# Kernel tuning notes

Hardware: AMD Instinct MI355X
Metric: run time of the kernel (lower is better)

The kernel has to match this reference:

```python
import jax, jax.numpy as jnp
import numpy as np


def _bilinear_grid_sample(fea, grid):
    """torch.nn.functional.grid_sample, mode=bilinear, padding_mode=zeros, align_corners=False.
    fea: (B,C,H,W); grid: (B,Hg,Wg,2) with xy in [-1,1]. Returns (B,C,Hg,Wg)."""
    B, C, H, W = fea.shape
    Hg, Wg = grid.shape[1], grid.shape[2]
    gx, gy = grid[..., 0], grid[..., 1]
    # unnormalize (align_corners=False)
    x = ((gx + 1.0) * W - 1.0) * 0.5
    y = ((gy + 1.0) * H - 1.0) * 0.5
    x0 = jnp.floor(x); y0 = jnp.floor(y)
    x1 = x0 + 1.0;     y1 = y0 + 1.0
    wx1 = x - x0; wx0 = 1.0 - wx1
    wy1 = y - y0; wy0 = 1.0 - wy1
    flat = fea.reshape(B, C, H * W)

    def corner(xi, yi, w):
        valid = (xi >= 0) & (xi <= W - 1) & (yi >= 0) & (yi <= H - 1)
        xi_c = jnp.clip(xi, 0, W - 1).astype(jnp.int32)
        yi_c = jnp.clip(yi, 0, H - 1).astype(jnp.int32)
        idx = (yi_c * W + xi_c).reshape(B, 1, Hg * Wg)
        v = jnp.take_along_axis(flat, jnp.broadcast_to(idx, (B, C, Hg * Wg)), axis=2)
        return v * (w * valid.astype(fea.dtype)).reshape(B, 1, Hg * Wg)

    out = (corner(x0, y0, wx0 * wy0) + corner(x1, y0, wx1 * wy0)
           + corner(x0, y1, wx0 * wy1) + corner(x1, y1, wx1 * wy1))
    return out.reshape(B, C, Hg, Wg)


def _conv1d_k1(x, W, b):
    # x: (B,Cin,N), W: (Cout,Cin), b: (Cout,) -> (B,Cout,N)
    return jnp.einsum('oc,bcn->bon', W, x) + b[None, :, None]


def setup_inputs() -> dict:
    key = jax.random.key(0)
    ks = jax.random.split(key, 8)
    B, C, H, W = 4, 16, 90, 160
    N_s, N_anchor, N_y = 8, 200, 20
    scale = 8
    fea = jax.random.normal(ks[0], (B, C, H, W), dtype=jnp.float32)
    sampled_3d_points = jax.random.normal(ks[1], (N_s, B, N_anchor, N_y, 4), dtype=jnp.float32)
    # 2D pixel coords at full resolution: x in [0, W*scale), y in [0, H*scale)
    u = jax.random.uniform(ks[2], (N_s, B, N_anchor, N_y, 2), dtype=jnp.float32)
    points_2d_coord = u * jnp.array([W * scale, H * scale], dtype=jnp.float32)
    W_local = jax.random.normal(ks[3], (16, 16), dtype=jnp.float32) * 0.25
    b_local = jax.random.normal(ks[4], (16,), dtype=jnp.float32) * 0.01
    W_emb = jax.random.normal(ks[5], (256, 4), dtype=jnp.float32) * 0.5
    b_emb = jax.random.normal(ks[6], (256,), dtype=jnp.float32) * 0.01
    return {"fea": fea, "sampled_3d_points": sampled_3d_points,
            "points_2d_coord": points_2d_coord,
            "W_local": W_local, "b_local": b_local,
            "W_emb": W_emb, "b_emb": b_emb, "scale": scale}


def reference(fea, sampled_3d_points, points_2d_coord, W_local, b_local, W_emb, b_emb, scale):
    B, C, H, W = fea.shape
    N_s, _, N_anchor, N_y, _ = points_2d_coord.shape
    # normalize 2D coords to [-1,1] grid
    norm_weight = jnp.array([1.0 / W, 1.0 / H], dtype=fea.dtype)
    ner = (points_2d_coord / scale) * norm_weight * 2.0 - 1.0
    ner = jnp.transpose(ner, (1, 0, 2, 3, 4)).reshape(B, N_s * N_anchor, N_y, 2)
    local_fea = _bilinear_grid_sample(fea, ner)            # (B,C,N_s*N_anchor,N_y)
    local_fea = local_fea.reshape(B, C, -1)                # (B,C,N)
    local_fea = _conv1d_k1(local_fea, W_local, b_local)    # (B,16,N)
    # point embedding: permute(1,4,0,2,3) -> (B,4,N_s,N_anchor,N_y)
    sp = jnp.transpose(sampled_3d_points, (1, 4, 0, 2, 3)).reshape(B, 4, -1)
    embedded_points = _conv1d_k1(sp, W_emb, b_emb)         # (B,256,N)
    return (embedded_points, local_fea)
```

## Files before the change

kernel.cpp:

```cpp
#include <hip/hip_runtime.h>

#define B_    4
#define C_    16
#define H_    90
#define W_    160
#define NS_   8
#define NA_   200
#define NY_   20
#define NPB_  (NS_*NA_*NY_)
#define NPB4_ (NPB_/4)
#define CO_   256
#define EMB_ELEMS ((size_t)B_*CO_*NPB_)
#define SCALE_F 8.0f
#define HW_   (H_*W_)

__global__ __launch_bounds__(256) void fused_local_emb_kernel(
    const float*  __restrict__ fea,
    const float4* __restrict__ sp3d,
    const float2* __restrict__ pc2d,
    const float*  __restrict__ W_local,
    const float*  __restrict__ b_local,
    const float4* __restrict__ W_emb,
    const float*  __restrict__ b_emb,
    float* __restrict__ out)
{
    __shared__ float4 sWe[CO_];
    __shared__ float  sbe[CO_];
    __shared__ float  sWl[256];
    __shared__ float  sbl[16];
    __shared__ float  sPx[256], sPy[256], sPz[256], sPw[256];
    __shared__ float  sV[16*256];

    const int tid = threadIdx.x;
    sWe[tid] = W_emb[tid];
    sbe[tid] = b_emb[tid];
    sWl[tid] = W_local[tid];
    if (tid < 16) sbl[tid] = b_local[tid];

    const int blk  = blockIdx.x;
    const int b    = blk / (NPB_/256);
    const int tile = blk % (NPB_/256);
    const int n    = tile*256 + tid;

    const int s   = n / (NA_*NY_);
    const int rem = n - s*(NA_*NY_);
    const int a   = rem / NY_;
    const int yy  = rem - a*NY_;

    const int pidx = ((s*B_ + b)*NA_ + a)*NY_ + yy;
    const float4 p  = sp3d[pidx];
    const float2 pc = pc2d[pidx];

    sPx[tid] = p.x; sPy[tid] = p.y; sPz[tid] = p.z; sPw[tid] = p.w;

    const float gx = (pc.x / SCALE_F) * (1.0f/(float)W_) * 2.0f - 1.0f;
    const float gy = (pc.y / SCALE_F) * (1.0f/(float)H_) * 2.0f - 1.0f;
    const float xf = ((gx + 1.0f) * (float)W_ - 1.0f) * 0.5f;
    const float yf = ((gy + 1.0f) * (float)H_ - 1.0f) * 0.5f;

    const float x0f = floorf(xf), y0f = floorf(yf);
    const float x1f = x0f + 1.0f, y1f = y0f + 1.0f;
    const float wx1 = xf - x0f, wx0 = 1.0f - wx1;
    const float wy1 = yf - y0f, wy0 = 1.0f - wy1;

    const float vx0 = (x0f >= 0.0f && x0f <= (float)(W_-1)) ? 1.0f : 0.0f;
    const float vx1 = (x1f >= 0.0f && x1f <= (float)(W_-1)) ? 1.0f : 0.0f;
    const float vy0 = (y0f >= 0.0f && y0f <= (float)(H_-1)) ? 1.0f : 0.0f;
    const float vy1 = (y1f >= 0.0f && y1f <= (float)(H_-1)) ? 1.0f : 0.0f;

    const int xi0 = (int)fminf(fmaxf(x0f, 0.0f), (float)(W_-1));
    const int xi1 = (int)fminf(fmaxf(x1f, 0.0f), (float)(W_-1));
    const int yi0 = (int)fminf(fmaxf(y0f, 0.0f), (float)(H_-1));
    const int yi1 = (int)fminf(fmaxf(y1f, 0.0f), (float)(H_-1));

    const float w00 = wx0*wy0*vx0*vy0;
    const float w01 = wx1*wy0*vx1*vy0;
    const float w10 = wx0*wy1*vx0*vy1;
    const float w11 = wx1*wy1*vx1*vy1;

    const int i00 = yi0*W_ + xi0;
    const int i01 = yi0*W_ + xi1;
    const int i10 = yi1*W_ + xi0;
    const int i11 = yi1*W_ + xi1;

    __syncthreads();

    const float* fb = fea + b*(C_*HW_);
    float f00[16], f01[16], f10[16], f11[16];
#pragma unroll
    for (int c = 0; c < 16; ++c) {
        const float* fc = fb + c*HW_;
        f00[c] = fc[i00];
        f01[c] = fc[i01];
        f10[c] = fc[i10];
        f11[c] = fc[i11];
    }

    const int l  = tid & 63;
    const int wv = tid >> 6;

    const float4 PX = ((const float4*)sPx)[l];
    const float4 PY = ((const float4*)sPy)[l];
    const float4 PZ = ((const float4*)sPz)[l];
    const float4 PW = ((const float4*)sPw)[l];

    float4* eo4 = (float4*)(out + (size_t)b*CO_*NPB_ + tile*256);
#pragma unroll
    for (int oi = 0; oi < 64; ++oi) {
        const int o = wv*64 + oi;
        const float4 w = sWe[o];
        const float bb = sbe[o];
        float4 r;
        r.x = fmaf(w.w, PW.x, fmaf(w.z, PZ.x, fmaf(w.y, PY.x, fmaf(w.x, PX.x, bb))));
        r.y = fmaf(w.w, PW.y, fmaf(w.z, PZ.y, fmaf(w.y, PY.y, fmaf(w.x, PX.y, bb))));
        r.z = fmaf(w.w, PW.z, fmaf(w.z, PZ.z, fmaf(w.y, PY.z, fmaf(w.x, PX.z, bb))));
        r.w = fmaf(w.w, PW.w, fmaf(w.z, PZ.w, fmaf(w.y, PY.w, fmaf(w.x, PX.w, bb))));
        eo4[o*NPB4_ + l] = r;
    }

    float v[16];
#pragma unroll
    for (int c = 0; c < 16; ++c)
        v[c] = w00*f00[c] + w01*f01[c] + w10*f10[c] + w11*f11[c];
#pragma unroll
    for (int c = 0; c < 16; ++c)
        sV[c*256 + tid] = v[c];

    __syncthreads();

    float4 acc[4];
#pragma unroll
    for (int k = 0; k < 4; ++k) {
        const float bk = sbl[4*wv + k];
        acc[k].x = bk; acc[k].y = bk; acc[k].z = bk; acc[k].w = bk;
    }
#pragma unroll
    for (int c = 0; c < 16; ++c) {
        const float4 sv = ((const float4*)(sV + c*256))[l];
#pragma unroll
        for (int k = 0; k < 4; ++k) {
            const float wl = sWl[(4*wv + k)*16 + c];
            acc[k].x = fmaf(wl, sv.x, acc[k].x);
            acc[k].y = fmaf(wl, sv.y, acc[k].y);
            acc[k].z = fmaf(wl, sv.z, acc[k].z);
            acc[k].w = fmaf(wl, sv.w, acc[k].w);
        }
    }
    float4* lo4 = (float4*)(out + EMB_ELEMS + (size_t)b*16*NPB_ + tile*256);
#pragma unroll
    for (int k = 0; k < 4; ++k)
        lo4[(4*wv + k)*NPB4_ + l] = acc[k];
}

extern "C" void kernel_launch(void* const* d_in, const int* in_sizes, int n_in,
                              void* d_out, int out_size, void* d_ws, size_t ws_size,
                              hipStream_t stream) {
    const float* fea     = (const float*)d_in[0];
    const float4* sp3d   = (const float4*)d_in[1];
    const float2* pc2d   = (const float2*)d_in[2];
    const float* W_local = (const float*)d_in[3];
    const float* b_local = (const float*)d_in[4];
    const float4* W_emb  = (const float4*)d_in[5];
    const float* b_emb   = (const float*)d_in[6];

    dim3 grid(B_ * (NPB_/256));
    dim3 block(256);
    fused_local_emb_kernel<<<grid, block, 0, stream>>>(
        fea, sp3d, pc2d, W_local, b_local, W_emb, b_emb, (float*)d_out);
}
```

Measured before the change: 39.90 us.

## Split embedding and grid-sample work into separate interleaved block roles

Blocks are now specialized: most compute the 256-channel point embedding for 4 output channels over a fifth of the points, while the rest do the bilinear grid-sample plus 16x16 conv. Embedding blocks read the 3D points straight from global memory, and the two block types are interleaved in the launch order so gather-heavy and store-heavy work run at the same time. This removes the shared-memory staging of embedding weights and points and the 64-iteration per-thread store loop from the gather blocks. In exchange, each embedding block rereads the point inputs, the block-index mapping is hardcoded (1500/1000), and the source-pointer expression contains an odd '*0' term.

```diff
diff --git a/kernel.cpp b/kernel.cpp
--- a/kernel.cpp
+++ b/kernel.cpp
@@ -14,6 +14,15 @@
 #define SCALE_F 8.0f
 #define HW_   (H_*W_)
 
+#define OC_PER_BLK 4
+#define NCHUNK     5
+#define NPC   (NPB_/NCHUNK)
+#define GPC   (NPC/4)
+#define STEPS (GPC/64)
+#define EMB_BLOCKS (B_*(CO_/OC_PER_BLK)*NCHUNK)
+#define LOC_BLOCKS (B_*NPB_/256)
+#define TOTAL_BLOCKS (EMB_BLOCKS + LOC_BLOCKS)
+
 __global__ __launch_bounds__(256) void fused_local_emb_kernel(
     const float*  __restrict__ fea,
     const float4* __restrict__ sp3d,
@@ -24,22 +33,58 @@
     const float*  __restrict__ b_emb,
     float* __restrict__ out)
 {
-    __shared__ float4 sWe[CO_];
-    __shared__ float  sbe[CO_];
-    __shared__ float  sWl[256];
-    __shared__ float  sbl[16];
-    __shared__ float  sPx[256], sPy[256], sPz[256], sPw[256];
-    __shared__ float  sV[16*256];
+    const int tid = threadIdx.x;
+    const int idx = blockIdx.x;
 
-    const int tid = threadIdx.x;
-    sWe[tid] = W_emb[tid];
-    sbe[tid] = b_emb[tid];
+    int emb_id = -1, loc_id = -1;
+    if (idx < 1500) {
+        const int grp = idx / 3, r = idx - grp*3;
+        if (r == 2) loc_id = grp;
+        else        emb_id = grp*2 + r;
+    } else {
+        emb_id = 1000 + (idx - 1500);
+    }
+
+    if (emb_id >= 0) {
+        const int b   = emb_id / ((CO_/OC_PER_BLK)*NCHUNK);
+        const int rem = emb_id - b*((CO_/OC_PER_BLK)*NCHUNK);
+        const int oc  = rem / NCHUNK;
+        const int nc  = rem - oc*NCHUNK;
+        const int wv  = tid >> 6, l = tid & 63;
+        const int o   = oc*OC_PER_BLK + wv;
+
+        const float4 w  = W_emb[o];
+        const float  bb = b_emb[o];
+
+        float4* row4 = (float4*)(out + (size_t)b*CO_*NPB_ + (size_t)o*NPB_) + nc*GPC;
+
+#pragma unroll 5
+        for (int st = 0; st < STEPS; ++st) {
+            const int g  = nc*GPC + st*64 + l;
+            const int s  = g / 1000;
+            const int gi = g - s*1000;
+            const float4* pb = sp3d + (s*(B_*NA_*NY_) + b*(NA_*NY_))/1 * 0
+                                    + s*(B_*NA_*NY_) + b*(NA_*NY_) + gi*4;
+            const float4 p0 = pb[0], p1 = pb[1], p2 = pb[2], p3 = pb[3];
+            float4 r;
+            r.x = fmaf(w.w,p0.w, fmaf(w.z,p0.z, fmaf(w.y,p0.y, fmaf(w.x,p0.x, bb))));
+            r.y = fmaf(w.w,p1.w, fmaf(w.z,p1.z, fmaf(w.y,p1.y, fmaf(w.x,p1.x, bb))));
+            r.z = fmaf(w.w,p2.w, fmaf(w.z,p2.z, fmaf(w.y,p2.y, fmaf(w.x,p2.x, bb))));
+            r.w = fmaf(w.w,p3.w, fmaf(w.z,p3.z, fmaf(w.y,p3.y, fmaf(w.x,p3.x, bb))));
+            row4[st*64 + l] = r;
+        }
+        return;
+    }
+
+    __shared__ float sWl[256];
+    __shared__ float sbl[16];
+    __shared__ float sV[16*256];
+
     sWl[tid] = W_local[tid];
     if (tid < 16) sbl[tid] = b_local[tid];
 
-    const int blk  = blockIdx.x;
-    const int b    = blk / (NPB_/256);
-    const int tile = blk % (NPB_/256);
+    const int b    = loc_id / (NPB_/256);
+    const int tile = loc_id - b*(NPB_/256);
     const int n    = tile*256 + tid;
 
     const int s   = n / (NA_*NY_);
@@ -48,10 +93,7 @@
     const int yy  = rem - a*NY_;
 
     const int pidx = ((s*B_ + b)*NA_ + a)*NY_ + yy;
-    const float4 p  = sp3d[pidx];
     const float2 pc = pc2d[pidx];
-
-    sPx[tid] = p.x; sPy[tid] = p.y; sPz[tid] = p.z; sPw[tid] = p.w;
 
     const float gx = (pc.x / SCALE_F) * (1.0f/(float)W_) * 2.0f - 1.0f;
     const float gy = (pc.y / SCALE_F) * (1.0f/(float)H_) * 2.0f - 1.0f;
@@ -83,8 +125,6 @@
     const int i10 = yi1*W_ + xi0;
     const int i11 = yi1*W_ + xi1;
 
-    __syncthreads();
-
     const float* fb = fea + b*(C_*HW_);
     float f00[16], f01[16], f10[16], f11[16];
 #pragma unroll
@@ -96,28 +136,6 @@
         f11[c] = fc[i11];
     }
 
-    const int l  = tid & 63;
-    const int wv = tid >> 6;
-
-    const float4 PX = ((const float4*)sPx)[l];
-    const float4 PY = ((const float4*)sPy)[l];
-    const float4 PZ = ((const float4*)sPz)[l];
-    const float4 PW = ((const float4*)sPw)[l];
-
-    float4* eo4 = (float4*)(out + (size_t)b*CO_*NPB_ + tile*256);
-#pragma unroll
-    for (int oi = 0; oi < 64; ++oi) {
-        const int o = wv*64 + oi;
-        const float4 w = sWe[o];
-        const float bb = sbe[o];
-        float4 r;
-        r.x = fmaf(w.w, PW.x, fmaf(w.z, PZ.x, fmaf(w.y, PY.x, fmaf(w.x, PX.x, bb))));
-        r.y = fmaf(w.w, PW.y, fmaf(w.z, PZ.y, fmaf(w.y, PY.y, fmaf(w.x, PX.y, bb))));
-        r.z = fmaf(w.w, PW.z, fmaf(w.z, PZ.z, fmaf(w.y, PY.z, fmaf(w.x, PX.z, bb))));
-        r.w = fmaf(w.w, PW.w, fmaf(w.z, PZ.w, fmaf(w.y, PY.w, fmaf(w.x, PX.w, bb))));
-        eo4[o*NPB4_ + l] = r;
-    }
-
     float v[16];
 #pragma unroll
     for (int c = 0; c < 16; ++c)
@@ -127,6 +145,9 @@
         sV[c*256 + tid] = v[c];
 
     __syncthreads();
+
+    const int l  = tid & 63;
+    const int wv = tid >> 6;
 
     float4 acc[4];
 #pragma unroll
@@ -163,7 +184,7 @@
     const float4* W_emb  = (const float4*)d_in[5];
     const float* b_emb   = (const float*)d_in[6];
 
-    dim3 grid(B_ * (NPB_/256));
+    dim3 grid(TOTAL_BLOCKS);
     dim3 block(256);
     fused_local_emb_kernel<<<grid, block, 0, stream>>>(
         fea, sp3d, pc2d, W_local, b_local, W_emb, b_emb, (float*)d_out);
```

Result: slower. 59.77 us (+49.8%).

## Split embedding and local-feature work into separate specialized blocks in one grid

Applied to the files above, without the earlier changes.

The fused kernel is split by block index into two roles. Local-feature blocks do the bilinear gather and the 16x16 projection. Embedding blocks each compute a quarter of the 256 output channels for one tile. This gives five times as many blocks, which should improve occupancy and spread the store-bound embedding writes across more CUs, and it lets gather latency overlap with other blocks' stores. A single unioned shared buffer reduces LDS use per block. In exchange, the sp3d point loads are repeated across the four channel chunks.

```diff
diff --git a/kernel.cpp b/kernel.cpp
--- a/kernel.cpp
+++ b/kernel.cpp
@@ -14,6 +14,14 @@
 #define SCALE_F 8.0f
 #define HW_   (H_*W_)
 
+#define TILES_    (NPB_/256)
+#define LOC_BLOCKS (B_*TILES_)
+#define OCHUNKS_  4
+#define EMB_BLOCKS (B_*TILES_*OCHUNKS_)
+#define TOTAL_BLOCKS (LOC_BLOCKS + EMB_BLOCKS)
+
+#define SMEM_FLOATS 4368
+
 __global__ __launch_bounds__(256) void fused_local_emb_kernel(
     const float*  __restrict__ fea,
     const float4* __restrict__ sp3d,
@@ -24,22 +32,71 @@
     const float*  __restrict__ b_emb,
     float* __restrict__ out)
 {
-    __shared__ float4 sWe[CO_];
-    __shared__ float  sbe[CO_];
-    __shared__ float  sWl[256];
-    __shared__ float  sbl[16];
-    __shared__ float  sPx[256], sPy[256], sPz[256], sPw[256];
-    __shared__ float  sV[16*256];
+    __shared__ float smem[SMEM_FLOATS];
+    const int tid = threadIdx.x;
+    const int idx = blockIdx.x;
+    const int l  = tid & 63;
+    const int wv = tid >> 6;
 
-    const int tid = threadIdx.x;
-    sWe[tid] = W_emb[tid];
-    sbe[tid] = b_emb[tid];
+    if (idx >= LOC_BLOCKS) {
+        const int eid  = idx - LOC_BLOCKS;
+        const int b    = eid / (TILES_*OCHUNKS_);
+        const int rem0 = eid - b*(TILES_*OCHUNKS_);
+        const int tile = rem0 / OCHUNKS_;
+        const int oc   = rem0 - tile*OCHUNKS_;
+
+        float* sPx = smem;
+        float* sPy = smem + 256;
+        float* sPz = smem + 512;
+        float* sPw = smem + 768;
+        float4* sWe4 = (float4*)(smem + 1024);
+        float*  sbe  = smem + 1280;
+
+        if (tid < 64) {
+            sWe4[tid] = W_emb[oc*64 + tid];
+            sbe[tid]  = b_emb[oc*64 + tid];
+        }
+
+        const int n   = tile*256 + tid;
+        const int s   = n / (NA_*NY_);
+        const int rem = n - s*(NA_*NY_);
+        const int a   = rem / NY_;
+        const int yy  = rem - a*NY_;
+        const float4 p = sp3d[((s*B_ + b)*NA_ + a)*NY_ + yy];
+        sPx[tid] = p.x; sPy[tid] = p.y; sPz[tid] = p.z; sPw[tid] = p.w;
+        __syncthreads();
+
+        const float4 PX = ((const float4*)sPx)[l];
+        const float4 PY = ((const float4*)sPy)[l];
+        const float4 PZ = ((const float4*)sPz)[l];
+        const float4 PW = ((const float4*)sPw)[l];
+
+        float4* eo4 = (float4*)(out + (size_t)b*CO_*NPB_);
+        const int obase = wv*16;
+        const int ostart = oc*64 + obase;
+#pragma unroll
+        for (int k = 0; k < 16; ++k) {
+            const float4 w = sWe4[obase + k];
+            const float bb = sbe[obase + k];
+            float4 r;
+            r.x = fmaf(w.w,PW.x, fmaf(w.z,PZ.x, fmaf(w.y,PY.x, fmaf(w.x,PX.x, bb))));
+            r.y = fmaf(w.w,PW.y, fmaf(w.z,PZ.y, fmaf(w.y,PY.y, fmaf(w.x,PX.y, bb))));
+            r.z = fmaf(w.w,PW.z, fmaf(w.z,PZ.z, fmaf(w.y,PY.z, fmaf(w.x,PX.z, bb))));
+            r.w = fmaf(w.w,PW.w, fmaf(w.z,PZ.w, fmaf(w.y,PY.w, fmaf(w.x,PX.w, bb))));
+            eo4[(size_t)(ostart + k)*NPB4_ + tile*64 + l] = r;
+        }
+        return;
+    }
+
+    float* sWl = smem;
+    float* sbl = smem + 256;
+    float* sV  = smem + 272;
+
     sWl[tid] = W_local[tid];
     if (tid < 16) sbl[tid] = b_local[tid];
 
-    const int blk  = blockIdx.x;
-    const int b    = blk / (NPB_/256);
-    const int tile = blk % (NPB_/256);
+    const int b    = idx / TILES_;
+    const int tile = idx - b*TILES_;
     const int n    = tile*256 + tid;
 
     const int s   = n / (NA_*NY_);
@@ -47,11 +104,7 @@
     const int a   = rem / NY_;
     const int yy  = rem - a*NY_;
 
-    const int pidx = ((s*B_ + b)*NA_ + a)*NY_ + yy;
-    const float4 p  = sp3d[pidx];
-    const float2 pc = pc2d[pidx];
-
-    sPx[tid] = p.x; sPy[tid] = p.y; sPz[tid] = p.z; sPw[tid] = p.w;
+    const float2 pc = pc2d[((s*B_ + b)*NA_ + a)*NY_ + yy];
 
     const float gx = (pc.x / SCALE_F) * (1.0f/(float)W_) * 2.0f - 1.0f;
     const float gy = (pc.y / SCALE_F) * (1.0f/(float)H_) * 2.0f - 1.0f;
@@ -83,8 +136,6 @@
     const int i10 = yi1*W_ + xi0;
     const int i11 = yi1*W_ + xi1;
 
-    __syncthreads();
-
     const float* fb = fea + b*(C_*HW_);
     float f00[16], f01[16], f10[16], f11[16];
 #pragma unroll
@@ -94,28 +145,6 @@
         f01[c] = fc[i01];
         f10[c] = fc[i10];
         f11[c] = fc[i11];
-    }
-
-    const int l  = tid & 63;
-    const int wv = tid >> 6;
-
-    const float4 PX = ((const float4*)sPx)[l];
-    const float4 PY = ((const float4*)sPy)[l];
-    const float4 PZ = ((const float4*)sPz)[l];
-    const float4 PW = ((const float4*)sPw)[l];
-
-    float4* eo4 = (float4*)(out + (size_t)b*CO_*NPB_ + tile*256);
-#pragma unroll
-    for (int oi = 0; oi < 64; ++oi) {
-        const int o = wv*64 + oi;
-        const float4 w = sWe[o];
-        const float bb = sbe[o];
-        float4 r;
-        r.x = fmaf(w.w, PW.x, fmaf(w.z, PZ.x, fmaf(w.y, PY.x, fmaf(w.x, PX.x, bb))));
-        r.y = fmaf(w.w, PW.y, fmaf(w.z, PZ.y, fmaf(w.y, PY.y, fmaf(w.x, PX.y, bb))));
-        r.z = fmaf(w.w, PW.z, fmaf(w.z, PZ.z, fmaf(w.y, PY.z, fmaf(w.x, PX.z, bb))));
-        r.w = fmaf(w.w, PW.w, fmaf(w.z, PZ.w, fmaf(w.y, PY.w, fmaf(w.x, PX.w, bb))));
-        eo4[o*NPB4_ + l] = r;
     }
 
     float v[16];
@@ -163,7 +192,7 @@
     const float4* W_emb  = (const float4*)d_in[5];
     const float* b_emb   = (const float*)d_in[6];
 
-    dim3 grid(B_ * (NPB_/256));
+    dim3 grid(TOTAL_BLOCKS);
     dim3 block(256);
     fused_local_emb_kernel<<<grid, block, 0, stream>>>(
         fea, sp3d, pc2d, W_local, b_local, W_emb, b_emb, (float*)d_out);
```

New measurement: 42.81 us. +7.3%, slower.
